# Performance work log

Measured on AMD Instinct MI355X. Metric: run time of the kernel, lower is better.

## Reference

```python
import jax, jax.numpy as jnp
import numpy as np

EPS = 1e-7
TOPK = 10
IOU_THR = 0.1
REG_W, OBJ_W, CLS_W = 5.0, 1.0, 1.0
NUM_CLASSES = 80
STRIDES = (8, 16, 32)


def _corners(b):
    cx, cy, w, h = b[..., 0], b[..., 1], b[..., 2], b[..., 3]
    return cx - w / 2, cy - h / 2, cx + w / 2, cy + h / 2


def bbox_iou(box1, box2, ciou=False):
    # boxes in (cx, cy, w, h); broadcastable shapes [..., 4]
    x11, y11, x12, y12 = _corners(box1)
    x21, y21, x22, y22 = _corners(box2)
    iw = jnp.clip(jnp.minimum(x12, x22) - jnp.maximum(x11, x21), 0)
    ih = jnp.clip(jnp.minimum(y12, y22) - jnp.maximum(y11, y21), 0)
    inter = iw * ih
    a1 = (x12 - x11) * (y12 - y11)
    a2 = (x22 - x21) * (y22 - y21)
    union = a1 + a2 - inter + EPS
    iou = inter / union
    if not ciou:
        return iou
    cw = jnp.maximum(x12, x22) - jnp.minimum(x11, x21)
    ch = jnp.maximum(y12, y22) - jnp.minimum(y11, y21)
    c2 = cw ** 2 + ch ** 2 + EPS
    rho2 = ((x21 + x22 - x11 - x12) ** 2 + (y21 + y22 - y11 - y12) ** 2) / 4
    v = 4 / 3.14159 ** 2 * (jnp.arctan((x22 - x21) / (y22 - y21 + EPS))
                            - jnp.arctan((x12 - x11) / (y12 - y11 + EPS))) ** 2
    alpha = jax.lax.stop_gradient(v / (1 - iou + v + EPS))
    return iou - (rho2 / c2 + v * alpha)


def _bce_logits(x, t):
    # BCEWithLogitsLoss, reduction='none' (numerically stable)
    return jnp.maximum(x, 0) - x * t + jnp.log1p(jnp.exp(-jnp.abs(x)))


def _flat(p):
    # [B, C, H, W] -> [B, H*W, C] matching permute(1,2,0).reshape(-1, C)
    B, C, H, W = p.shape
    return p.transpose(0, 2, 3, 1).reshape(B, H * W, C)


def _grids(shapes):
    gs, ss = [], []
    for (H, W), s in zip(shapes, STRIDES):
        yv, xv = jnp.meshgrid(jnp.arange(H), jnp.arange(W), indexing='ij')
        gs.append(jnp.stack([xv, yv], -1).astype(jnp.float32).reshape(-1, 2))
        ss.append(jnp.full((H * W,), float(s), dtype=jnp.float32))
    return jnp.concatenate(gs, 0), jnp.concatenate(ss, 0)


def _yolox_loss(p3_cls, p3_reg, p3_obj, p4_cls, p4_reg, p4_obj,
                p5_cls, p5_reg, p5_obj, targets):
    B = p3_cls.shape[0]
    shapes = [p3_cls.shape[2:], p4_cls.shape[2:], p5_cls.shape[2:]]
    grids, strides = _grids(shapes)            # [A,2], [A]
    cls_preds = jnp.concatenate([_flat(p3_cls), _flat(p4_cls), _flat(p5_cls)], 1)  # [B,A,C]
    reg_preds = jnp.concatenate([_flat(p3_reg), _flat(p4_reg), _flat(p5_reg)], 1)  # [B,A,4]
    obj_preds = jnp.concatenate([_flat(p3_obj), _flat(p4_obj), _flat(p5_obj)], 1)[..., 0]  # [B,A]
    A = cls_preds.shape[1]

    # decode predicted boxes (cx, cy, w, h) in image coords
    pred_cx = (grids[:, 0] + jax.nn.sigmoid(reg_preds[..., 0])) * strides
    pred_cy = (grids[:, 1] + jax.nn.sigmoid(reg_preds[..., 1])) * strides
    pred_w = jnp.exp(reg_preds[..., 2]) * strides
    pred_h = jnp.exp(reg_preds[..., 3]) * strides
    pred_boxes = jnp.stack([pred_cx, pred_cy, pred_w, pred_h], -1)  # [B,A,4]

    # targets: (x, y, w, h, class) with x,y top-left -> center format
    t_cx = targets[..., 0] + targets[..., 2] / 2
    t_cy = targets[..., 1] + targets[..., 3] / 2
    tboxes = jnp.stack([t_cx, t_cy, targets[..., 2], targets[..., 3]], -1)  # [B,T,4]
    tcls = targets[..., 4].astype(jnp.int32)  # [B,T]

    # SimOTA-style candidate selection: top-k closest anchor centers per target
    ac = grids * strides[:, None] + strides[:, None] / 2  # [A,2]
    dist = jnp.sqrt((ac[None, None, :, 0] - t_cx[..., None]) ** 2
                    + (ac[None, None, :, 1] - t_cy[..., None]) ** 2)  # [B,T,A]
    _, idx = jax.lax.top_k(-dist, TOPK)  # [B,T,K] smallest distances

    bidx = jnp.arange(B)[:, None, None]
    sel_boxes = pred_boxes[bidx, idx]                           # [B,T,K,4]
    ious = bbox_iou(sel_boxes, tboxes[:, :, None, :])           # [B,T,K]
    valid = ious > IOU_THR
    has_valid = valid.any(-1, keepdims=True)
    fallback = jnp.arange(TOPK) == jnp.argmax(ious, -1)[..., None]
    amask = jnp.where(has_valid, valid, fallback)               # [B,T,K] bool
    w = amask.astype(jnp.float32)
    num_pos = jnp.maximum(w.sum(), 1.0)

    cious = bbox_iou(sel_boxes, tboxes[:, :, None, :], ciou=True)
    reg_sum = ((1.0 - cious) * w).sum()

    # classification loss at assigned anchors
    sel_cls = cls_preds[bidx, idx]                              # [B,T,K,C]
    onehot = jax.nn.one_hot(tcls, NUM_CLASSES, dtype=jnp.float32)[:, :, None, :]
    cls_sum = (_bce_logits(sel_cls, onehot).sum(-1) * w).sum()

    # objectness: target 1 at any assigned anchor (scatter-max), 0 elsewhere
    obj_t = jnp.zeros((B, A), jnp.float32).at[bidx, idx].max(w)
    obj_sum = _bce_logits(obj_preds, obj_t).sum()

    reg_l = reg_sum / num_pos
    obj_l = obj_sum / num_pos
    cls_l = cls_sum / num_pos
    total = REG_W * reg_l + OBJ_W * obj_l + CLS_W * cls_l
    return jnp.stack([total, reg_l, obj_l, cls_l])


def setup_inputs() -> dict:
    key = jax.random.key(0)
    ks = jax.random.split(key, 12)
    B, T = 32, 50
    d = {}
    shapes = {'p3': (80, 80), 'p4': (40, 40), 'p5': (20, 20)}
    i = 0
    for name, (H, W) in shapes.items():
        d[f'{name}_cls'] = jax.random.normal(ks[i], (B, NUM_CLASSES, H, W), jnp.float32); i += 1
        d[f'{name}_reg'] = jax.random.normal(ks[i], (B, 4, H, W), jnp.float32); i += 1
        d[f'{name}_obj'] = jax.random.normal(ks[i], (B, 1, H, W), jnp.float32); i += 1
    xy = jax.random.uniform(ks[9], (B, T, 2)) * 500.0
    wh = jax.random.uniform(ks[10], (B, T, 2)) * 120.0 + 8.0
    cls_id = jax.random.randint(ks[11], (B, T, 1), 0, NUM_CLASSES).astype(jnp.float32)
    d['targets'] = jnp.concatenate([xy, wh, cls_id], -1)
    return d


def reference(p3_cls, p3_reg, p3_obj, p4_cls, p4_reg, p4_obj,
              p5_cls, p5_reg, p5_obj, targets):
    return _yolox_loss(p3_cls, p3_reg, p3_obj, p4_cls, p4_reg, p4_obj,
                       p5_cls, p5_reg, p5_obj, targets)
```

## Files before the change

kernel.cpp:

```cpp
#include <hip/hip_runtime.h>
#include <math.h>

#define B 32
#define T 50
#define KK 10
#define NC 80
#define A_TOT 8400
#define EPSF 1e-7f
#define IOU_THR 0.1f

#define WORDS_PER_B 264
#define BITS_BYTES (B * WORDS_PER_B * 4)

__device__ __forceinline__ float softplus_bce0(float x) {
    return fmaxf(x, 0.0f) + log1pf(expf(-fabsf(x)));
}

__device__ __forceinline__ void decode_level(int a, int& aa, int& W, int& HW, float& s) {
    if (a < 6400)      { aa = a;        W = 80; HW = 6400; s = 8.0f;  }
    else if (a < 8000) { aa = a - 6400; W = 40; HW = 1600; s = 16.0f; }
    else               { aa = a - 8000; W = 20; HW = 400;  s = 32.0f; }
}

__device__ __forceinline__ void csw(float& da, int& ia, float& db, int& ib) {
    if (db < da || (db == da && ib < ia)) {
        float td = da; da = db; db = td;
        int ti = ia; ia = ib; ib = ti;
    }
}

__global__ __launch_bounds__(64) void fused_kernel(
    const float* __restrict__ c3, const float* __restrict__ r3,
    const float* __restrict__ c4, const float* __restrict__ r4,
    const float* __restrict__ c5, const float* __restrict__ r5,
    const float* __restrict__ o3, const float* __restrict__ o4,
    const float* __restrict__ o5, const float* __restrict__ targets,
    unsigned int* __restrict__ bits, float4* __restrict__ partials)
{
    int bt = blockIdx.x;
    int b = bt / T;
    int lane = threadIdx.x;
    const float* tg = targets + bt * 5;
    float tw = tg[2], th = tg[3];
    float tcx = tg[0] + tw * 0.5f, tcy = tg[1] + th * 0.5f;
    int tcls = (int)tg[4];

    int ci = lane & 7, ri = lane >> 3;

    float d0, d1, d2; int id0, id1, id2;
    {
        int j0 = (int)(tcx * 0.125f), i0 = (int)(tcy * 0.125f);
        int js = min(max(j0 - 3, 0), 72), is = min(max(i0 - 3, 0), 72);
        int j = js + ci, i = is + ri;
        float dx = j * 8.0f + 4.0f - tcx, dy = i * 8.0f + 4.0f - tcy;
        d0 = sqrtf(dx * dx + dy * dy); id0 = i * 80 + j;
    }
    {
        int j0 = (int)(tcx * 0.0625f), i0 = (int)(tcy * 0.0625f);
        int js = min(max(j0 - 3, 0), 32), is = min(max(i0 - 3, 0), 32);
        int j = js + ci, i = is + ri;
        float dx = j * 16.0f + 8.0f - tcx, dy = i * 16.0f + 8.0f - tcy;
        d1 = sqrtf(dx * dx + dy * dy); id1 = 6400 + i * 40 + j;
    }
    {
        int j0 = (int)(tcx * 0.03125f), i0 = (int)(tcy * 0.03125f);
        int js = min(max(j0 - 3, 0), 12), is = min(max(i0 - 3, 0), 12);
        int j = js + ci, i = is + ri;
        float dx = j * 32.0f + 16.0f - tcx, dy = i * 32.0f + 16.0f - tcy;
        d2 = sqrtf(dx * dx + dy * dy); id2 = 8000 + i * 20 + j;
    }
    csw(d0, id0, d1, id1);
    csw(d1, id1, d2, id2);
    csw(d0, id0, d1, id1);

    int a = 0;
    for (int k = 0; k < KK; ++k) {
        float bd = d0; int bid = id0;
#pragma unroll
        for (int sft = 1; sft < 64; sft <<= 1) {
            float od = __shfl_xor(bd, sft);
            int oid  = __shfl_xor(bid, sft);
            if (od < bd || (od == bd && oid < bid)) { bd = od; bid = oid; }
        }
        if (d0 == bd && id0 == bid) {
            d0 = d1; id0 = id1;
            d1 = d2; id1 = id2;
            d2 = INFINITY; id2 = 0x7fffffff;
        }
        if (lane == k) a = bid;
    }

    float x21 = tcx - tw * 0.5f, y21 = tcy - th * 0.5f;
    float x22 = tcx + tw * 0.5f, y22 = tcy + th * 0.5f;

    float iou = -INFINITY, ciou = 0.0f;
    bool valid = false;
    if (lane < KK) {
        int aa, W, HW; float s;
        decode_level(a, aa, W, HW, s);
        int i = aa / W, j = aa - i * W;
        const float* rb = (HW == 6400) ? r3 : (HW == 1600 ? r4 : r5);
        size_t rbase = ((size_t)b * 4) * (size_t)HW + (size_t)aa;
        float r0 = rb[rbase];
        float r1 = rb[rbase + (size_t)HW];
        float r2 = rb[rbase + 2 * (size_t)HW];
        float r3v = rb[rbase + 3 * (size_t)HW];
        float px = ((float)j + 1.0f / (1.0f + expf(-r0))) * s;
        float py = ((float)i + 1.0f / (1.0f + expf(-r1))) * s;
        float pw = expf(r2) * s;
        float ph = expf(r3v) * s;
        float x11 = px - pw * 0.5f, y11 = py - ph * 0.5f;
        float x12 = px + pw * 0.5f, y12 = py + ph * 0.5f;
        float iw = fmaxf(fminf(x12, x22) - fmaxf(x11, x21), 0.0f);
        float ih = fmaxf(fminf(y12, y22) - fmaxf(y11, y21), 0.0f);
        float inter = iw * ih;
        float a1 = (x12 - x11) * (y12 - y11);
        float a2 = (x22 - x21) * (y22 - y21);
        float uni = a1 + a2 - inter + EPSF;
        iou = inter / uni;
        valid = iou > IOU_THR;
        float cw = fmaxf(x12, x22) - fminf(x11, x21);
        float ch = fmaxf(y12, y22) - fminf(y11, y21);
        float c2 = cw * cw + ch * ch + EPSF;
        float ddx = x21 + x22 - x11 - x12;
        float ddy = y21 + y22 - y11 - y12;
        float rho2 = (ddx * ddx + ddy * ddy) * 0.25f;
        const float CPI = (float)(4.0 / (3.14159 * 3.14159));
        float dat = atanf((x22 - x21) / (y22 - y21 + EPSF))
                  - atanf((x12 - x11) / (y12 - y11 + EPSF));
        float v = CPI * dat * dat;
        float alpha = v / (1.0f - iou + v + EPSF);
        ciou = iou - (rho2 / c2 + v * alpha);
    }

    unsigned long long vmask = __ballot(valid);
    bool has_valid = (vmask != 0ull);

    float bi = iou; int bl = lane;
#pragma unroll
    for (int sft = 1; sft < 64; sft <<= 1) {
        float oi = __shfl_xor(bi, sft);
        int ol  = __shfl_xor(bl, sft);
        if (oi > bi || (oi == bi && ol < bl)) { bi = oi; bl = ol; }
    }

    bool w = (lane < KK) && (has_valid ? valid : (lane == bl));
    unsigned long long wmask0 = __ballot(w);
    int npcount = __popcll(wmask0);

    float regc = w ? (1.0f - ciou) : 0.0f;
#pragma unroll
    for (int sft = 1; sft < 64; sft <<= 1) regc += __shfl_xor(regc, sft);

    float osum = 0.0f;
    {
        int gt = bt * 64 + lane;
        osum += softplus_bce0(o3[gt]);
        osum += softplus_bce0(o3[gt + 102400]);
        if (gt < 51200) osum += softplus_bce0(o4[gt]);
        if (gt < 12800) osum += softplus_bce0(o5[gt]);
    }
    if (w) {
        unsigned int bit = 1u << (a & 31);
        unsigned int old = atomicOr(&bits[b * WORDS_PER_B + (a >> 5)], bit);
        if (!(old & bit)) {
            int aa, W, HW; float s;
            decode_level(a, aa, W, HW, s);
            const float* ob = (HW == 6400) ? o3 : (HW == 1600 ? o4 : o5);
            osum -= ob[(size_t)b * HW + aa];
        }
    }
#pragma unroll
    for (int sft = 1; sft < 64; sft <<= 1) osum += __shfl_xor(osum, sft);

    float csum = 0.0f;
    unsigned long long wmask = wmask0;
    while (wmask) {
        int k = __ffsll(wmask) - 1;
        wmask &= wmask - 1;
        int ak = __shfl(a, k);
        int aak, Wk, HWk; float sk;
        decode_level(ak, aak, Wk, HWk, sk);
        const float* cb = (HWk == 6400) ? c3 : (HWk == 1600 ? c4 : c5);
        size_t cbase = ((size_t)b * NC) * (size_t)HWk + (size_t)aak;
        csum += softplus_bce0(cb[cbase + (size_t)lane * HWk]);
        if (lane < NC - 64)
            csum += softplus_bce0(cb[cbase + (size_t)(64 + lane) * HWk]);
        if (lane == 0)
            csum -= cb[cbase + (size_t)tcls * HWk];
    }
#pragma unroll
    for (int sft = 1; sft < 64; sft <<= 1) csum += __shfl_xor(csum, sft);

    if (lane == 0)
        partials[bt] = make_float4(regc, csum, (float)npcount, osum);
}

__global__ __launch_bounds__(256) void finalize_kernel(
    const float4* __restrict__ partials, float* __restrict__ out)
{
    int tid = threadIdx.x;
    float reg = 0.0f, cls = 0.0f, np = 0.0f, obj = 0.0f;
    for (int i = tid; i < B * T; i += 256) {
        float4 p = partials[i];
        reg += p.x; cls += p.y; np += p.z; obj += p.w;
    }
#pragma unroll
    for (int sft = 1; sft < 64; sft <<= 1) {
        reg += __shfl_xor(reg, sft);
        cls += __shfl_xor(cls, sft);
        np  += __shfl_xor(np, sft);
        obj += __shfl_xor(obj, sft);
    }
    __shared__ float sred[4][4];
    int wv = tid >> 6;
    if ((tid & 63) == 0) {
        sred[wv][0] = reg; sred[wv][1] = cls; sred[wv][2] = np; sred[wv][3] = obj;
    }
    __syncthreads();
    if (tid == 0) {
        float R = 0, C = 0, N = 0, O = 0;
        for (int i = 0; i < 4; ++i) {
            R += sred[i][0]; C += sred[i][1]; N += sred[i][2]; O += sred[i][3];
        }
        float npf = fmaxf(N, 1.0f);
        float reg_l = R / npf, cls_l = C / npf, obj_l = O / npf;
        out[0] = 5.0f * reg_l + obj_l + cls_l;
        out[1] = reg_l;
        out[2] = obj_l;
        out[3] = cls_l;
    }
}

extern "C" void kernel_launch(void* const* d_in, const int* in_sizes, int n_in,
                              void* d_out, int out_size, void* d_ws, size_t ws_size,
                              hipStream_t stream) {
    const float* p3c = (const float*)d_in[0];
    const float* p3r = (const float*)d_in[1];
    const float* p3o = (const float*)d_in[2];
    const float* p4c = (const float*)d_in[3];
    const float* p4r = (const float*)d_in[4];
    const float* p4o = (const float*)d_in[5];
    const float* p5c = (const float*)d_in[6];
    const float* p5r = (const float*)d_in[7];
    const float* p5o = (const float*)d_in[8];
    const float* targets = (const float*)d_in[9];

    char* ws = (char*)d_ws;
    unsigned int* bits = (unsigned int*)ws;
    float4* partials = (float4*)(ws + BITS_BYTES);

    hipMemsetAsync(bits, 0, BITS_BYTES, stream);

    fused_kernel<<<B * T, 64, 0, stream>>>(p3c, p3r, p4c, p4r, p5c, p5r,
                                           p3o, p4o, p5o, targets,
                                           bits, partials);
    finalize_kernel<<<1, 256, 0, stream>>>(partials, (float*)d_out);
}
```

Baseline: 139.5 us.

## Pack top-k keys into 64-bit and flatten class-loss gathers across lanes

Distance and index are packed into one 64-bit key, so the top-k wave reductions compare a single value. The objectness loads are issued at kernel start so their latency overlaps the assignment work. The per-winner serial class loop becomes a flat item space of winners times classes, with up to four gathers issued up front through a shared-memory anchor list. This aims to expose more memory-level parallelism and cut serial latency, at the cost of more registers, a __syncthreads and 64-bit shuffles.

```diff
diff --git a/kernel.cpp b/kernel.cpp
--- a/kernel.cpp
+++ b/kernel.cpp
@@ -22,11 +22,12 @@
     else               { aa = a - 8000; W = 20; HW = 400;  s = 32.0f; }
 }
 
-__device__ __forceinline__ void csw(float& da, int& ia, float& db, int& ib) {
-    if (db < da || (db == da && ib < ia)) {
-        float td = da; da = db; db = td;
-        int ti = ia; ia = ib; ib = ti;
-    }
+__device__ __forceinline__ unsigned long long pack_key(float d, int id) {
+    return ((unsigned long long)__float_as_uint(d) << 32) | (unsigned int)id;
+}
+
+__device__ __forceinline__ void cswk(unsigned long long& ka, unsigned long long& kb) {
+    if (kb < ka) { unsigned long long t = ka; ka = kb; kb = t; }
 }
 
 __global__ __launch_bounds__(64) void fused_kernel(
@@ -40,6 +41,13 @@
     int bt = blockIdx.x;
     int b = bt / T;
     int lane = threadIdx.x;
+
+    int gt = bt * 64 + lane;
+    float ov0 = o3[gt];
+    float ov1 = o3[gt + 102400];
+    float ov2 = (gt < 51200) ? o4[gt] : 0.0f;
+    float ov3 = (gt < 12800) ? o5[gt] : 0.0f;
+
     const float* tg = targets + bt * 5;
     float tw = tg[2], th = tg[3];
     float tcx = tg[0] + tw * 0.5f, tcy = tg[1] + th * 0.5f;
@@ -47,47 +55,42 @@
 
     int ci = lane & 7, ri = lane >> 3;
 
-    float d0, d1, d2; int id0, id1, id2;
+    unsigned long long k0, k1, k2;
     {
         int j0 = (int)(tcx * 0.125f), i0 = (int)(tcy * 0.125f);
         int js = min(max(j0 - 3, 0), 72), is = min(max(i0 - 3, 0), 72);
         int j = js + ci, i = is + ri;
         float dx = j * 8.0f + 4.0f - tcx, dy = i * 8.0f + 4.0f - tcy;
-        d0 = sqrtf(dx * dx + dy * dy); id0 = i * 80 + j;
+        k0 = pack_key(sqrtf(dx * dx + dy * dy), i * 80 + j);
     }
     {
         int j0 = (int)(tcx * 0.0625f), i0 = (int)(tcy * 0.0625f);
         int js = min(max(j0 - 3, 0), 32), is = min(max(i0 - 3, 0), 32);
         int j = js + ci, i = is + ri;
         float dx = j * 16.0f + 8.0f - tcx, dy = i * 16.0f + 8.0f - tcy;
-        d1 = sqrtf(dx * dx + dy * dy); id1 = 6400 + i * 40 + j;
+        k1 = pack_key(sqrtf(dx * dx + dy * dy), 6400 + i * 40 + j);
     }
     {
         int j0 = (int)(tcx * 0.03125f), i0 = (int)(tcy * 0.03125f);
         int js = min(max(j0 - 3, 0), 12), is = min(max(i0 - 3, 0), 12);
         int j = js + ci, i = is + ri;
         float dx = j * 32.0f + 16.0f - tcx, dy = i * 32.0f + 16.0f - tcy;
-        d2 = sqrtf(dx * dx + dy * dy); id2 = 8000 + i * 20 + j;
-    }
-    csw(d0, id0, d1, id1);
-    csw(d1, id1, d2, id2);
-    csw(d0, id0, d1, id1);
+        k2 = pack_key(sqrtf(dx * dx + dy * dy), 8000 + i * 20 + j);
+    }
+    cswk(k0, k1); cswk(k1, k2); cswk(k0, k1);
 
     int a = 0;
     for (int k = 0; k < KK; ++k) {
-        float bd = d0; int bid = id0;
+        unsigned long long bk = k0;
 #pragma unroll
         for (int sft = 1; sft < 64; sft <<= 1) {
-            float od = __shfl_xor(bd, sft);
-            int oid  = __shfl_xor(bid, sft);
-            if (od < bd || (od == bd && oid < bid)) { bd = od; bid = oid; }
-        }
-        if (d0 == bd && id0 == bid) {
-            d0 = d1; id0 = id1;
-            d1 = d2; id1 = id2;
-            d2 = INFINITY; id2 = 0x7fffffff;
-        }
-        if (lane == k) a = bid;
+            unsigned long long ok = __shfl_xor(bk, sft);
+            if (ok < bk) bk = ok;
+        }
+        if (k0 == bk) {
+            k0 = k1; k1 = k2; k2 = ~0ull;
+        }
+        if (lane == k) a = (int)(unsigned int)(bk & 0xffffffffull);
     }
 
     float x21 = tcx - tw * 0.5f, y21 = tcy - th * 0.5f;
@@ -146,54 +149,77 @@
 
     bool w = (lane < KK) && (has_valid ? valid : (lane == bl));
     unsigned long long wmask0 = __ballot(w);
-    int npcount = __popcll(wmask0);
+    int nw = __popcll(wmask0);
 
     float regc = w ? (1.0f - ciou) : 0.0f;
 #pragma unroll
     for (int sft = 1; sft < 64; sft <<= 1) regc += __shfl_xor(regc, sft);
 
-    float osum = 0.0f;
-    {
-        int gt = bt * 64 + lane;
-        osum += softplus_bce0(o3[gt]);
-        osum += softplus_bce0(o3[gt + 102400]);
-        if (gt < 51200) osum += softplus_bce0(o4[gt]);
-        if (gt < 12800) osum += softplus_bce0(o5[gt]);
-    }
+    unsigned int oldbits = 0, bit = 0;
     if (w) {
-        unsigned int bit = 1u << (a & 31);
-        unsigned int old = atomicOr(&bits[b * WORDS_PER_B + (a >> 5)], bit);
-        if (!(old & bit)) {
-            int aa, W, HW; float s;
-            decode_level(a, aa, W, HW, s);
-            const float* ob = (HW == 6400) ? o3 : (HW == 1600 ? o4 : o5);
-            osum -= ob[(size_t)b * HW + aa];
-        }
-    }
-#pragma unroll
-    for (int sft = 1; sft < 64; sft <<= 1) osum += __shfl_xor(osum, sft);
-
-    float csum = 0.0f;
-    unsigned long long wmask = wmask0;
-    while (wmask) {
-        int k = __ffsll(wmask) - 1;
-        wmask &= wmask - 1;
-        int ak = __shfl(a, k);
+        bit = 1u << (a & 31);
+        oldbits = atomicOr(&bits[b * WORDS_PER_B + (a >> 5)], bit);
+    }
+
+    __shared__ int s_aid[16];
+    if (w) {
+        int rank = __popcll(wmask0 & ((1ull << lane) - 1ull));
+        s_aid[rank] = a;
+    }
+    __syncthreads();
+    int n_items = nw * NC;
+
+    auto cls_ptr = [&](int item, int& c) -> const float* {
+        int k = item / NC;
+        c = item - k * NC;
+        int ak = s_aid[k];
         int aak, Wk, HWk; float sk;
         decode_level(ak, aak, Wk, HWk, sk);
         const float* cb = (HWk == 6400) ? c3 : (HWk == 1600 ? c4 : c5);
-        size_t cbase = ((size_t)b * NC) * (size_t)HWk + (size_t)aak;
-        csum += softplus_bce0(cb[cbase + (size_t)lane * HWk]);
-        if (lane < NC - 64)
-            csum += softplus_bce0(cb[cbase + (size_t)(64 + lane) * HWk]);
-        if (lane == 0)
-            csum -= cb[cbase + (size_t)tcls * HWk];
+        return cb + ((size_t)b * NC + (size_t)c) * (size_t)HWk + (size_t)aak;
+    };
+
+    bool m0 = lane < n_items;
+    bool m1 = 64 + lane < n_items;
+    bool m2 = 128 + lane < n_items;
+    bool m3 = 192 + lane < n_items;
+    int cc0 = 0, cc1 = 0, cc2 = 0, cc3 = 0;
+    float v0 = 0.0f, v1 = 0.0f, v2 = 0.0f, v3 = 0.0f;
+    if (m0) v0 = *cls_ptr(lane, cc0);
+    if (m1) v1 = *cls_ptr(64 + lane, cc1);
+    if (m2) v2 = *cls_ptr(128 + lane, cc2);
+    if (m3) v3 = *cls_ptr(192 + lane, cc3);
+
+    float osum = softplus_bce0(ov0) + softplus_bce0(ov1);
+    if (gt < 51200) osum += softplus_bce0(ov2);
+    if (gt < 12800) osum += softplus_bce0(ov3);
+    if (w && !(oldbits & bit)) {
+        int aa, W, HW; float s;
+        decode_level(a, aa, W, HW, s);
+        const float* ob = (HW == 6400) ? o3 : (HW == 1600 ? o4 : o5);
+        osum -= ob[(size_t)b * HW + aa];
+    }
+#pragma unroll
+    for (int sft = 1; sft < 64; sft <<= 1) osum += __shfl_xor(osum, sft);
+
+    float csum = 0.0f;
+    if (m0) csum += softplus_bce0(v0) - (cc0 == tcls ? v0 : 0.0f);
+    if (m1) csum += softplus_bce0(v1) - (cc1 == tcls ? v1 : 0.0f);
+    if (m2) csum += softplus_bce0(v2) - (cc2 == tcls ? v2 : 0.0f);
+    if (m3) csum += softplus_bce0(v3) - (cc3 == tcls ? v3 : 0.0f);
+    for (int base = 256; base < n_items; base += 64) {
+        int item = base + lane;
+        if (item < n_items) {
+            int c;
+            float v = *cls_ptr(item, c);
+            csum += softplus_bce0(v) - (c == tcls ? v : 0.0f);
+        }
     }
 #pragma unroll
     for (int sft = 1; sft < 64; sft <<= 1) csum += __shfl_xor(csum, sft);
 
     if (lane == 0)
-        partials[bt] = make_float4(regc, csum, (float)npcount, osum);
+        partials[bt] = make_float4(regc, csum, (float)nw, osum);
 }
 
 __global__ __launch_bounds__(256) void finalize_kernel(
```

New measurement: 133.5 us. 1.04x faster.
